# Optimization experiments

Measured on AMD Instinct MI355X. Metric: run time of the kernel, lower is better.

Reference implementation:

```python
import math
import jax, jax.numpy as jnp
import numpy as np

LMAX = 2


def _cg_complex(j1, m1, j2, m2, j3, m3):
    # Standard (Racah) Clebsch-Gordan coefficient <j1 m1 j2 m2 | j3 m3> for integer l.
    if m1 + m2 != m3 or j3 < abs(j1 - j2) or j3 > j1 + j2:
        return 0.0
    f = math.factorial
    pre = math.sqrt((2 * j3 + 1) * f(j3 + j1 - j2) * f(j3 - j1 + j2) * f(j1 + j2 - j3) / f(j1 + j2 + j3 + 1))
    pre *= math.sqrt(f(j3 + m3) * f(j3 - m3) * f(j1 - m1) * f(j1 + m1) * f(j2 - m2) * f(j2 + m2))
    kmin = max(0, j2 - j3 - m1, j1 + m2 - j3)
    kmax = min(j1 + j2 - j3, j1 - m1, j2 + m2)
    s = 0.0
    for k in range(kmin, kmax + 1):
        s += (-1.0) ** k / (f(k) * f(j1 + j2 - j3 - k) * f(j1 - m1 - k) * f(j2 + m2 - k) * f(j3 - j2 + m1 + k) * f(j3 - j1 - m2 + k))
    return pre * s


def _u_matrix(l):
    # Unitary map from complex SH (Condon-Shortley) to real SH, rows = real mu, cols = complex m.
    U = np.zeros((2 * l + 1, 2 * l + 1), dtype=np.complex128)
    U[l, l] = 1.0
    isq2 = 1.0 / math.sqrt(2.0)
    for m in range(1, l + 1):
        U[l + m, l - m] = isq2
        U[l + m, l + m] = ((-1.0) ** m) * isq2
        U[l - m, l - m] = 1j * isq2
        U[l - m, l + m] = -1j * ((-1.0) ** m) * isq2
    return U


def _real_clebsch_gordan(lmax):
    # Dense real-SH CG tensor over combined s=(l,m) indices, shape [S,S,S], S=(lmax+1)^2.
    S = (lmax + 1) ** 2
    cg = np.zeros((S, S, S))
    for l1 in range(lmax + 1):
        for l2 in range(lmax + 1):
            for l3 in range(abs(l1 - l2), min(lmax, l1 + l2) + 1):
                blk = np.zeros((2 * l1 + 1, 2 * l2 + 1, 2 * l3 + 1))
                for i1, m1 in enumerate(range(-l1, l1 + 1)):
                    for i2, m2 in enumerate(range(-l2, l2 + 1)):
                        for i3, m3 in enumerate(range(-l3, l3 + 1)):
                            blk[i1, i2, i3] = _cg_complex(l1, m1, l2, m2, l3, m3)
                U1, U2, U3 = _u_matrix(l1), _u_matrix(l2), _u_matrix(l3)
                r = np.einsum('am,bn,co,mno->abc', U1, U2, U3.conj(), blk.astype(np.complex128))
                r = r.real if (l1 + l2 + l3) % 2 == 0 else r.imag  # parity-dependent real part
                cg[l1 * l1:(l1 + 1) ** 2, l2 * l2:(l2 + 1) ** 2, l3 * l3:(l3 + 1) ** 2] = r
    return cg


def _sparse_cg(lmax):
    cg = _real_clebsch_gordan(lmax)
    i1, i2, i3 = np.nonzero(np.abs(cg) > 1e-10)
    vals = cg[i1, i2, i3].astype(np.float32)
    widx = np.floor(np.sqrt(i3.astype(np.float64))).astype(np.int32)  # l of output combined index
    return vals, i1.astype(np.int32), i2.astype(np.int32), i3.astype(np.int32), widx


def _spherical_harmonics_l2(d):
    # Real SH up to l=2, 'component' normalization (|x|=1 assumed). Order: (l,m) = (0,0),(1,-1),(1,0),(1,1),(2,-2..2).
    x, y, z = d[..., 0], d[..., 1], d[..., 2]
    s3, s5, s15 = math.sqrt(3.0), math.sqrt(5.0), math.sqrt(15.0)
    return jnp.stack([
        jnp.ones_like(x),
        s3 * y, s3 * z, s3 * x,
        s15 * x * y, s15 * y * z, 0.5 * s5 * (3.0 * z * z - 1.0), s15 * x * z, 0.5 * s15 * (x * x - y * y),
    ], axis=-1)


def setup_inputs():
    N_ATOMS, N_EDGES, N_BASIS, N_RADIAL = 1200, 12000, 128, 20
    S = (LMAX + 1) ** 2
    key = jax.random.key(0)
    ks = jax.random.split(key, 8)
    vals, i1, i2, i3, widx = _sparse_cg(LMAX)
    return {
        'x': jax.random.normal(ks[0], (N_ATOMS, S, N_BASIS), jnp.float32),
        'radial_ij': jax.random.uniform(ks[1], (N_EDGES, N_RADIAL), jnp.float32),
        'dir_ij': jax.random.normal(ks[2], (N_EDGES, 3), jnp.float32),
        'cutoff_ij': jax.random.uniform(ks[3], (N_EDGES, 1), jnp.float32),
        'W_filter': jax.random.normal(ks[6], (N_RADIAL, N_BASIS * (LMAX + 1)), jnp.float32) / math.sqrt(N_RADIAL),
        'b_filter': jnp.zeros((N_BASIS * (LMAX + 1),), jnp.float32),
        'cg_vals': jnp.asarray(vals),
        'idx_i': jax.random.randint(ks[4], (N_EDGES,), 0, N_ATOMS),
        'idx_j': jax.random.randint(ks[5], (N_EDGES,), 0, N_ATOMS),
        'cg_idx_in1': jnp.asarray(i1),
        'cg_idx_in2': jnp.asarray(i2),
        'cg_idx_out': jnp.asarray(i3),
        'w_idx': jnp.asarray(widx),
    }


def reference(x, radial_ij, dir_ij, cutoff_ij, W_filter, b_filter, cg_vals,
              idx_i, idx_j, cg_idx_in1, cg_idx_in2, cg_idx_out, w_idx):
    n_atoms, S, F = x.shape
    E = dir_ij.shape[0]
    d = dir_ij / jnp.linalg.norm(dir_ij, axis=-1, keepdims=True)
    Y = _spherical_harmonics_l2(d)                        # [E, S]
    Wij = (radial_ij @ W_filter + b_filter) * cutoff_ij   # [E, (lmax+1)*F]
    Wij = Wij.reshape(E, LMAX + 1, F)                     # per-l radial filter
    xj = x[idx_j]                                         # [E, S, F] neighbor features
    # Sparse CG tensor-product contraction over combined (l,m) indices.
    v = (Y[:, cg_idx_in2, None] * cg_vals[None, :, None]
         * Wij[:, w_idx, :] * xj[:, cg_idx_in1, :])       # [E, n_cg, F]
    yij = jnp.zeros((E, S, F), v.dtype).at[:, cg_idx_out, :].add(v)
    return jax.ops.segment_sum(yij, idx_i, num_segments=n_atoms)
```

## Files before the change

### kernel.cpp

```cpp
#include <hip/hip_runtime.h>
#include <math.h>


#define S9     9
#define MROW   12
#define MSZ    (S9 * MROW)
#define NF     128
#define NRAD   20
#define CAP    32
#define ROWF   (S9 * NF)

__device__ inline float2 f2fma(float a, float2 b, float2 c) {
    return make_float2(fmaf(a, b.x, c.x), fmaf(a, b.y, c.y));
}

__global__ __launch_bounds__(256) void prep_kernel(
    const int* __restrict__ idx_i, int E, int A,
    int* __restrict__ cnt,
    int* __restrict__ pos)
{
    int e = blockIdx.x * 256 + threadIdx.x;
    if (e < E) {
        int a = idx_i[e];
        int p = atomicAdd(&cnt[a], 1);
        pos[e] = (p < CAP) ? (a * CAP + p) : (A * CAP);
    }
}

__global__ __launch_bounds__(256) void so3_edge_slots(
    const float* __restrict__ x,
    const float* __restrict__ radial,
    const float* __restrict__ dir,
    const float* __restrict__ cutoff,
    const float* __restrict__ Wf,
    const float* __restrict__ bf,
    const float* __restrict__ cg_vals,
    const int* __restrict__ idx_j,
    const int* __restrict__ cg_i1,
    const int* __restrict__ cg_i2,
    const int* __restrict__ cg_i3,
    int ncg, int E,
    const int* __restrict__ pos,
    float* __restrict__ slots)
{
    const int wid  = threadIdx.x >> 6;
    const int lane = threadIdx.x & 63;
    const int e = blockIdx.x * 4 + wid;
    if (e >= E) return;

    __shared__ __align__(16) float Msh[4][MSZ];
    __shared__ float Ysh[4][S9];

    if (lane < 27) ((float4*)&Msh[wid][0])[lane] = make_float4(0.f, 0.f, 0.f, 0.f);

    float dx = dir[3 * e], dy = dir[3 * e + 1], dz = dir[3 * e + 2];
    const float inv = rsqrtf(dx * dx + dy * dy + dz * dz);
    dx *= inv; dy *= inv; dz *= inv;
    if (lane == 0) {
        const float s3c  = 1.7320508075688772f;
        const float s5c  = 2.2360679774997896f;
        const float s15c = 3.8729833462074170f;
        Ysh[wid][0] = 1.0f;
        Ysh[wid][1] = s3c * dy;
        Ysh[wid][2] = s3c * dz;
        Ysh[wid][3] = s3c * dx;
        Ysh[wid][4] = s15c * dx * dy;
        Ysh[wid][5] = s15c * dy * dz;
        Ysh[wid][6] = 0.5f * s5c * (3.0f * dz * dz - 1.0f);
        Ysh[wid][7] = s15c * dx * dz;
        Ysh[wid][8] = 0.5f * s15c * (dx * dx - dy * dy);
    }

    for (int k = lane; k < ncg; k += 64) {
        atomicAdd(&Msh[wid][cg_i3[k] * MROW + cg_i1[k]],
                  cg_vals[k] * Ysh[wid][cg_i2[k]]);
    }

    float rad[NRAD];
    #pragma unroll
    for (int r = 0; r < NRAD; ++r) rad[r] = radial[(size_t)e * NRAD + r];
    const float cut = cutoff[e];

    float2 w0 = ((const float2*)(bf + 0 * NF))[lane];
    float2 w1 = ((const float2*)(bf + 1 * NF))[lane];
    float2 w2 = ((const float2*)(bf + 2 * NF))[lane];
    #pragma unroll 4
    for (int r = 0; r < NRAD; ++r) {
        const float2* wrow = (const float2*)(Wf + r * (3 * NF));
        w0 = f2fma(rad[r], wrow[lane],       w0);
        w1 = f2fma(rad[r], wrow[lane + 64],  w1);
        w2 = f2fma(rad[r], wrow[lane + 128], w2);
    }
    w0.x *= cut; w0.y *= cut;
    w1.x *= cut; w1.y *= cut;
    w2.x *= cut; w2.y *= cut;

    const int j = __builtin_amdgcn_readfirstlane(idx_j[e]);
    const float2* xp = (const float2*)(x + (size_t)j * ROWF) + lane;
    float2 xj[S9];
    #pragma unroll
    for (int s = 0; s < S9; ++s) xj[s] = xp[s * 64];

    const int row = __builtin_amdgcn_readfirstlane(pos[e]);
    float2* sp = (float2*)(slots) + (size_t)row * (ROWF / 2) + lane;

    #pragma unroll
    for (int s3 = 0; s3 < S9; ++s3) {
        const float4* mr = (const float4*)&Msh[wid][s3 * MROW];
        const float4 m0 = mr[0];
        const float4 m1 = mr[1];
        const float  m8 = Msh[wid][s3 * MROW + 8];
        float2 tsum = make_float2(0.f, 0.f);
        tsum = f2fma(m0.x, xj[0], tsum);
        tsum = f2fma(m0.y, xj[1], tsum);
        tsum = f2fma(m0.z, xj[2], tsum);
        tsum = f2fma(m0.w, xj[3], tsum);
        tsum = f2fma(m1.x, xj[4], tsum);
        tsum = f2fma(m1.y, xj[5], tsum);
        tsum = f2fma(m1.z, xj[6], tsum);
        tsum = f2fma(m1.w, xj[7], tsum);
        tsum = f2fma(m8,   xj[8], tsum);
        const float2 wl = (s3 == 0) ? w0 : ((s3 < 4) ? w1 : w2);
        sp[s3 * 64] = make_float2(wl.x * tsum.x, wl.y * tsum.y);
    }
}

__global__ __launch_bounds__(256) void reduce_kernel(
    const float* __restrict__ slots, const int* __restrict__ cnt, int A,
    float* __restrict__ out)
{
    const int wid  = threadIdx.x >> 6;
    const int lane = threadIdx.x & 63;
    const int a  = blockIdx.x * 2 + (wid >> 1);
    const int sh = wid & 1;
    if (a >= A) return;
    const int deg = min(cnt[a], CAP);
    const int s0 = sh ? 5 : 0;
    const int ns = sh ? 4 : 5;

    float2 acc[5];
    #pragma unroll
    for (int s = 0; s < 5; ++s) acc[s] = make_float2(0.f, 0.f);

    const float2* base = (const float2*)(slots) + (size_t)a * CAP * (ROWF / 2) + lane;
    for (int p = 0; p < deg; ++p) {
        const float2* rp = base + (size_t)p * (ROWF / 2) + s0 * 64;
        #pragma unroll
        for (int s = 0; s < 5; ++s) {
            if (s < ns) {
                float2 v = rp[s * 64];
                acc[s].x += v.x; acc[s].y += v.y;
            }
        }
    }
    float2* op = (float2*)(out + (size_t)a * ROWF) + s0 * 64 + lane;
    #pragma unroll
    for (int s = 0; s < 5; ++s)
        if (s < ns) op[s * 64] = acc[s];
}

__global__ __launch_bounds__(256) void so3_edge_fused(
    const float* __restrict__ x, const float* __restrict__ radial,
    const float* __restrict__ dir, const float* __restrict__ cutoff,
    const float* __restrict__ Wf, const float* __restrict__ bf,
    const float* __restrict__ cg_vals,
    const int* __restrict__ idx_i, const int* __restrict__ idx_j,
    const int* __restrict__ cg_i1, const int* __restrict__ cg_i2,
    const int* __restrict__ cg_i3, int ncg, int E,
    float* __restrict__ out)
{
    const int wid  = threadIdx.x >> 6;
    const int lane = threadIdx.x & 63;
    const int e = blockIdx.x * 4 + wid;
    if (e >= E) return;

    __shared__ __align__(16) float Msh[4][MSZ];
    __shared__ float Ysh[4][S9];

    if (lane < 27) ((float4*)&Msh[wid][0])[lane] = make_float4(0.f, 0.f, 0.f, 0.f);

    float dx = dir[3 * e], dy = dir[3 * e + 1], dz = dir[3 * e + 2];
    const float inv = rsqrtf(dx * dx + dy * dy + dz * dz);
    dx *= inv; dy *= inv; dz *= inv;
    if (lane == 0) {
        const float s3c = 1.7320508075688772f, s5c = 2.2360679774997896f,
                    s15c = 3.8729833462074170f;
        Ysh[wid][0] = 1.0f;
        Ysh[wid][1] = s3c * dy; Ysh[wid][2] = s3c * dz; Ysh[wid][3] = s3c * dx;
        Ysh[wid][4] = s15c * dx * dy; Ysh[wid][5] = s15c * dy * dz;
        Ysh[wid][6] = 0.5f * s5c * (3.0f * dz * dz - 1.0f);
        Ysh[wid][7] = s15c * dx * dz;
        Ysh[wid][8] = 0.5f * s15c * (dx * dx - dy * dy);
    }
    for (int k = lane; k < ncg; k += 64)
        atomicAdd(&Msh[wid][cg_i3[k] * MROW + cg_i1[k]], cg_vals[k] * Ysh[wid][cg_i2[k]]);

    float rad[NRAD];
    #pragma unroll
    for (int r = 0; r < NRAD; ++r) rad[r] = radial[(size_t)e * NRAD + r];
    const float cut = cutoff[e];

    float2 w0 = ((const float2*)(bf + 0 * NF))[lane];
    float2 w1 = ((const float2*)(bf + 1 * NF))[lane];
    float2 w2 = ((const float2*)(bf + 2 * NF))[lane];
    #pragma unroll 4
    for (int r = 0; r < NRAD; ++r) {
        const float2* wrow = (const float2*)(Wf + r * (3 * NF));
        w0 = f2fma(rad[r], wrow[lane], w0);
        w1 = f2fma(rad[r], wrow[lane + 64], w1);
        w2 = f2fma(rad[r], wrow[lane + 128], w2);
    }
    w0.x *= cut; w0.y *= cut; w1.x *= cut; w1.y *= cut; w2.x *= cut; w2.y *= cut;

    const int j = __builtin_amdgcn_readfirstlane(idx_j[e]);
    const float2* xp = (const float2*)(x + (size_t)j * ROWF) + lane;
    float2 xj[S9];
    #pragma unroll
    for (int s = 0; s < S9; ++s) xj[s] = xp[s * 64];

    const int a = __builtin_amdgcn_readfirstlane(idx_i[e]);
    float* op = out + (size_t)a * ROWF + 2 * lane;
    #pragma unroll
    for (int s3 = 0; s3 < S9; ++s3) {
        const float4* mr = (const float4*)&Msh[wid][s3 * MROW];
        const float4 m0 = mr[0];
        const float4 m1 = mr[1];
        const float  m8 = Msh[wid][s3 * MROW + 8];
        float2 tsum = make_float2(0.f, 0.f);
        tsum = f2fma(m0.x, xj[0], tsum);
        tsum = f2fma(m0.y, xj[1], tsum);
        tsum = f2fma(m0.z, xj[2], tsum);
        tsum = f2fma(m0.w, xj[3], tsum);
        tsum = f2fma(m1.x, xj[4], tsum);
        tsum = f2fma(m1.y, xj[5], tsum);
        tsum = f2fma(m1.z, xj[6], tsum);
        tsum = f2fma(m1.w, xj[7], tsum);
        tsum = f2fma(m8,   xj[8], tsum);
        const float2 wl = (s3 == 0) ? w0 : ((s3 < 4) ? w1 : w2);
        atomicAdd(&op[s3 * NF],     wl.x * tsum.x);
        atomicAdd(&op[s3 * NF + 1], wl.y * tsum.y);
    }
}

extern "C" void kernel_launch(void* const* d_in, const int* in_sizes, int n_in,
                              void* d_out, int out_size, void* d_ws, size_t ws_size,
                              hipStream_t stream) {
    const float* x       = (const float*)d_in[0];
    const float* radial  = (const float*)d_in[1];
    const float* dir     = (const float*)d_in[2];
    const float* cutoff  = (const float*)d_in[3];
    const float* Wf      = (const float*)d_in[4];
    const float* bf      = (const float*)d_in[5];
    const float* cg_vals = (const float*)d_in[6];
    const int*   idx_i   = (const int*)d_in[7];
    const int*   idx_j   = (const int*)d_in[8];
    const int*   cg_i1   = (const int*)d_in[9];
    const int*   cg_i2   = (const int*)d_in[10];
    const int*   cg_i3   = (const int*)d_in[11];

    const int E   = in_sizes[7];
    const int ncg = in_sizes[6];
    const int A   = in_sizes[0] / ROWF;

    int* cnt = (int*)d_ws;
    int* pos = cnt + A;
    size_t ib   = (size_t)(A + E) * sizeof(int);
    size_t soff = (ib + 255) & ~(size_t)255;
    float* slots = (float*)((char*)d_ws + soff);
    size_t need = soff + ((size_t)A * CAP + 1) * ROWF * sizeof(float);

    if (ws_size >= need) {
        hipMemsetAsync(cnt, 0, (size_t)A * sizeof(int), stream);

        prep_kernel<<<(E + 255) / 256, 256, 0, stream>>>(idx_i, E, A, cnt, pos);

        so3_edge_slots<<<(E + 3) / 4, 256, 0, stream>>>(
            x, radial, dir, cutoff, Wf, bf, cg_vals, idx_j,
            cg_i1, cg_i2, cg_i3, ncg, E, pos, slots);

        reduce_kernel<<<(A + 1) / 2, 256, 0, stream>>>(slots, cnt, A, (float*)d_out);
    } else {
        hipMemsetAsync(d_out, 0, (size_t)out_size * sizeof(float), stream);
        so3_edge_fused<<<(E + 3) / 4, 256, 0, stream>>>(
            x, radial, dir, cutoff, Wf, bf, cg_vals, idx_i, idx_j,
            cg_i1, cg_i2, cg_i3, ncg, E, (float*)d_out);
    }
}
```

Measured before the change: 132.5 us.

## Fold slot assignment into edge kernel and split atom reduction across waves

Removes the separate prep kernel. Each edge wave now claims its slot with an atomicAdd on the per-atom counter and broadcasts the row index, so the pos buffer and one launch go away. The edge kernel handles 8 edges per 512-thread block instead of 4 per 256. The reduce kernel now gives one block per atom, with four waves striding over the neighbor slots and combining their partial sums through shared memory, instead of two waves per atom each covering part of the feature rows.

```diff
diff --git a/kernel.cpp b/kernel.cpp
--- a/kernel.cpp
+++ b/kernel.cpp
@@ -9,25 +9,13 @@
 #define NRAD   20
 #define CAP    32
 #define ROWF   (S9 * NF)
+#define EPB    8
 
 __device__ inline float2 f2fma(float a, float2 b, float2 c) {
     return make_float2(fmaf(a, b.x, c.x), fmaf(a, b.y, c.y));
 }
 
-__global__ __launch_bounds__(256) void prep_kernel(
-    const int* __restrict__ idx_i, int E, int A,
-    int* __restrict__ cnt,
-    int* __restrict__ pos)
-{
-    int e = blockIdx.x * 256 + threadIdx.x;
-    if (e < E) {
-        int a = idx_i[e];
-        int p = atomicAdd(&cnt[a], 1);
-        pos[e] = (p < CAP) ? (a * CAP + p) : (A * CAP);
-    }
-}
-
-__global__ __launch_bounds__(256) void so3_edge_slots(
+__global__ __launch_bounds__(512) void so3_edge_slots(
     const float* __restrict__ x,
     const float* __restrict__ radial,
     const float* __restrict__ dir,
@@ -35,21 +23,30 @@
     const float* __restrict__ Wf,
     const float* __restrict__ bf,
     const float* __restrict__ cg_vals,
+    const int* __restrict__ idx_i,
     const int* __restrict__ idx_j,
     const int* __restrict__ cg_i1,
     const int* __restrict__ cg_i2,
     const int* __restrict__ cg_i3,
-    int ncg, int E,
-    const int* __restrict__ pos,
+    int ncg, int E, int A,
+    int* __restrict__ cnt,
     float* __restrict__ slots)
 {
     const int wid  = threadIdx.x >> 6;
     const int lane = threadIdx.x & 63;
-    const int e = blockIdx.x * 4 + wid;
+    const int e = blockIdx.x * EPB + wid;
     if (e >= E) return;
 
-    __shared__ __align__(16) float Msh[4][MSZ];
-    __shared__ float Ysh[4][S9];
+    __shared__ __align__(16) float Msh[EPB][MSZ];
+    __shared__ float Ysh[EPB][S9];
+
+    int row = 0;
+    if (lane == 0) {
+        const int a = idx_i[e];
+        const int p = atomicAdd(&cnt[a], 1);
+        row = (p < CAP) ? (a * CAP + p) : (A * CAP);
+    }
+    row = __shfl(row, 0);
 
     if (lane < 27) ((float4*)&Msh[wid][0])[lane] = make_float4(0.f, 0.f, 0.f, 0.f);
 
@@ -101,7 +98,6 @@
     #pragma unroll
     for (int s = 0; s < S9; ++s) xj[s] = xp[s * 64];
 
-    const int row = __builtin_amdgcn_readfirstlane(pos[e]);
     float2* sp = (float2*)(slots) + (size_t)row * (ROWF / 2) + lane;
 
     #pragma unroll
@@ -126,37 +122,50 @@
 }
 
 __global__ __launch_bounds__(256) void reduce_kernel(
-    const float* __restrict__ slots, const int* __restrict__ cnt, int A,
+    const float* __restrict__ slots, const int* __restrict__ cnt,
     float* __restrict__ out)
 {
+    const int a    = blockIdx.x;
     const int wid  = threadIdx.x >> 6;
     const int lane = threadIdx.x & 63;
-    const int a  = blockIdx.x * 2 + (wid >> 1);
-    const int sh = wid & 1;
-    if (a >= A) return;
     const int deg = min(cnt[a], CAP);
-    const int s0 = sh ? 5 : 0;
-    const int ns = sh ? 4 : 5;
-
-    float2 acc[5];
-    #pragma unroll
-    for (int s = 0; s < 5; ++s) acc[s] = make_float2(0.f, 0.f);
+
+    __shared__ float red[3][ROWF];
+
+    float2 acc[S9];
+    #pragma unroll
+    for (int s = 0; s < S9; ++s) acc[s] = make_float2(0.f, 0.f);
 
     const float2* base = (const float2*)(slots) + (size_t)a * CAP * (ROWF / 2) + lane;
-    for (int p = 0; p < deg; ++p) {
-        const float2* rp = base + (size_t)p * (ROWF / 2) + s0 * 64;
-        #pragma unroll
-        for (int s = 0; s < 5; ++s) {
-            if (s < ns) {
-                float2 v = rp[s * 64];
+    for (int p = wid; p < deg; p += 4) {
+        const float2* rp = base + (size_t)p * (ROWF / 2);
+        #pragma unroll
+        for (int s = 0; s < S9; ++s) {
+            float2 v = rp[s * 64];
+            acc[s].x += v.x; acc[s].y += v.y;
+        }
+    }
+
+    if (wid > 0) {
+        float2* rp = (float2*)&red[wid - 1][0];
+        #pragma unroll
+        for (int s = 0; s < S9; ++s) rp[s * 64 + lane] = acc[s];
+    }
+    __syncthreads();
+    if (wid == 0) {
+        #pragma unroll
+        for (int r2 = 0; r2 < 3; ++r2) {
+            const float2* rp = (const float2*)&red[r2][0];
+            #pragma unroll
+            for (int s = 0; s < S9; ++s) {
+                float2 v = rp[s * 64 + lane];
                 acc[s].x += v.x; acc[s].y += v.y;
             }
         }
-    }
-    float2* op = (float2*)(out + (size_t)a * ROWF) + s0 * 64 + lane;
-    #pragma unroll
-    for (int s = 0; s < 5; ++s)
-        if (s < ns) op[s * 64] = acc[s];
+        float2* op = (float2*)(out + (size_t)a * ROWF) + lane;
+        #pragma unroll
+        for (int s = 0; s < S9; ++s) op[s * 64] = acc[s];
+    }
 }
 
 __global__ __launch_bounds__(256) void so3_edge_fused(
@@ -263,22 +272,18 @@
     const int A   = in_sizes[0] / ROWF;
 
     int* cnt = (int*)d_ws;
-    int* pos = cnt + A;
-    size_t ib   = (size_t)(A + E) * sizeof(int);
-    size_t soff = (ib + 255) & ~(size_t)255;
+    size_t soff = (((size_t)A * sizeof(int)) + 255) & ~(size_t)255;
     float* slots = (float*)((char*)d_ws + soff);
     size_t need = soff + ((size_t)A * CAP + 1) * ROWF * sizeof(float);
 
     if (ws_size >= need) {
         hipMemsetAsync(cnt, 0, (size_t)A * sizeof(int), stream);
 
-        prep_kernel<<<(E + 255) / 256, 256, 0, stream>>>(idx_i, E, A, cnt, pos);
-
-        so3_edge_slots<<<(E + 3) / 4, 256, 0, stream>>>(
-            x, radial, dir, cutoff, Wf, bf, cg_vals, idx_j,
-            cg_i1, cg_i2, cg_i3, ncg, E, pos, slots);
-
-        reduce_kernel<<<(A + 1) / 2, 256, 0, stream>>>(slots, cnt, A, (float*)d_out);
+        so3_edge_slots<<<(E + EPB - 1) / EPB, 64 * EPB, 0, stream>>>(
+            x, radial, dir, cutoff, Wf, bf, cg_vals, idx_i, idx_j,
+            cg_i1, cg_i2, cg_i3, ncg, E, A, cnt, slots);
+
+        reduce_kernel<<<A, 256, 0, stream>>>(slots, cnt, (float*)d_out);
     } else {
         hipMemsetAsync(d_out, 0, (size_t)out_size * sizeof(float), stream);
         so3_edge_fused<<<(E + 3) / 4, 256, 0, stream>>>(
```

New measurement: 128.7 us. 1.03x faster.
